# Kernel optimization log

Measured on AMD Instinct MI355X. Metric: run time of the kernel, lower is better.

## Reference

```python
import jax, jax.numpy as jnp
import numpy as np

NUM_SLOTS = 8
SLOT_DIM = 256
ITERS = 3
EPS = 1e-8
SCALE = SLOT_DIM ** -0.5


def _ln(x, g, b, eps=1e-5):
    m = jnp.mean(x, axis=-1, keepdims=True)
    v = jnp.mean(jnp.square(x - m), axis=-1, keepdims=True)
    return (x - m) * jax.lax.rsqrt(v + eps) * g + b


def setup_inputs() -> dict:
    key = jax.random.key(0)
    ks = jax.random.split(key, 16)
    b, n, c = 32, 1024, 256
    d = SLOT_DIM
    def xavier(k, shape):
        fan_in, fan_out = shape[1], shape[0]
        lim = np.sqrt(6.0 / (fan_in + fan_out))
        return jax.random.uniform(k, shape, jnp.float32, -lim, lim)
    lim_mu = np.sqrt(6.0 / (1 + d))
    return {
        "inputs": jax.random.normal(ks[0], (b, n, c), jnp.float32),
        "noise": jax.random.normal(ks[1], (b, NUM_SLOTS, d), jnp.float32),
        "slots_mu": jax.random.uniform(ks[2], (1, 1, d), jnp.float32, -lim_mu, lim_mu),
        "slots_log_sigma": jax.random.uniform(ks[3], (1, 1, d), jnp.float32, -lim_mu, lim_mu),
        "Wq": xavier(ks[4], (d, d)),
        "Wk": xavier(ks[5], (d, c)),
        "Wv": xavier(ks[6], (d, c)),
        "gru_wih": xavier(ks[7], (3 * d, d)),
        "gru_whh": xavier(ks[8], (3 * d, d)),
        "gru_bih": jnp.zeros((3 * d,), jnp.float32),
        "gru_bhh": jnp.zeros((3 * d,), jnp.float32),
        "mlp_w1": xavier(ks[9], (4 * d, d)),
        "mlp_b1": jnp.zeros((4 * d,), jnp.float32),
        "mlp_w2": xavier(ks[10], (d, 4 * d)),
        "mlp_b2": jnp.zeros((d,), jnp.float32),
        "ln_in_g": jnp.ones((c,), jnp.float32),
        "ln_in_b": jnp.zeros((c,), jnp.float32),
        "ln_s_g": jnp.ones((d,), jnp.float32),
        "ln_s_b": jnp.zeros((d,), jnp.float32),
        "ln_ff_g": jnp.ones((d,), jnp.float32),
        "ln_ff_b": jnp.zeros((d,), jnp.float32),
    }


def reference(inputs, noise, slots_mu, slots_log_sigma, Wq, Wk, Wv,
              gru_wih, gru_whh, gru_bih, gru_bhh,
              mlp_w1, mlp_b1, mlp_w2, mlp_b2,
              ln_in_g, ln_in_b, ln_s_g, ln_s_b, ln_ff_g, ln_ff_b):
    b = inputs.shape[0]
    d = SLOT_DIM
    # slots ~ N(mu, sigma) reparameterized with given noise
    slots = slots_mu + jnp.exp(slots_log_sigma) * noise  # [b, S, d]
    x = _ln(inputs, ln_in_g, ln_in_b)
    k = jnp.einsum('bnc,dc->bnd', x, Wk)
    v = jnp.einsum('bnc,dc->bnd', x, Wv)
    for _ in range(ITERS):
        slots_prev = slots
        s = _ln(slots, ln_s_g, ln_s_b)
        q = jnp.einsum('bid,ed->bie', s, Wq)
        dots = jnp.einsum('bid,bjd->bij', q, k) * SCALE  # [b, S, n]
        attn = jax.nn.softmax(dots, axis=1) + EPS         # softmax over slots
        attn = attn / jnp.sum(attn, axis=-1, keepdims=True)
        updates = jnp.einsum('bjd,bij->bid', v, attn)      # [b, S, d]
        # GRUCell: x=updates, h=slots_prev (flattened over batch*slots)
        u = updates.reshape(-1, d)
        h = slots_prev.reshape(-1, d)
        gi = u @ gru_wih.T + gru_bih
        gh = h @ gru_whh.T + gru_bhh
        i_r, i_z, i_n = jnp.split(gi, 3, axis=-1)
        h_r, h_z, h_n = jnp.split(gh, 3, axis=-1)
        r = jax.nn.sigmoid(i_r + h_r)
        z = jax.nn.sigmoid(i_z + h_z)
        nn_ = jnp.tanh(i_n + r * h_n)
        slots = ((1.0 - z) * nn_ + z * h).reshape(b, -1, d)
        ff = _ln(slots, ln_ff_g, ln_ff_b)
        ff = jax.nn.relu(ff @ mlp_w1.T + mlp_b1) @ mlp_w2.T + mlp_b2
        slots = slots + ff
    return slots
```

## Files before the change

### kernel.cpp

```cpp
#include <hip/hip_runtime.h>


typedef __attribute__((ext_vector_type(8))) __bf16 bf16x8;
typedef __attribute__((ext_vector_type(4))) float  f32x4;

#define MFMA16(a, b, c) __builtin_amdgcn_mfma_f32_16x16x32_bf16((a), (b), (c), 0, 0, 0)

static __device__ __forceinline__ unsigned short f2bf(float f) {
    unsigned int x = __float_as_uint(f);
    x = (x + 0x7fffu + ((x >> 16) & 1u)) >> 16;
    return (unsigned short)x;
}
static __device__ __forceinline__ float bf2f(unsigned short u) {
    return __uint_as_float((unsigned int)u << 16);
}
static __device__ __forceinline__ float bflo(unsigned int x) {
    return __uint_as_float(x << 16);
}
static __device__ __forceinline__ float bfhi(unsigned int x) {
    return __uint_as_float(x & 0xffff0000u);
}

struct Params {
    const float *inputs, *noise, *mu, *ls;
    const float *Wq, *Wk, *Wv, *wih, *whh, *bih, *bhh, *w1, *b1, *w2, *b2;
    const float *ln_in_g, *ln_in_b, *ln_s_g, *ln_s_b, *ln_ff_g, *ln_ff_b;
    float* out;
    unsigned short *x_bf, *kvW_bf, *Wq_bf, *wih_bf, *whh_bf, *w1_bf, *w2_bf;
    unsigned short *kv_bf, *h_bf, *ff_bf, *h1_bf;
    float *slots, *q, *upart, *rspart, *gi, *gh, *opart;
};

static __device__ void qgemm(const Params& p, const unsigned short (&u)[16][264], int r0) {
    const int t = threadIdx.x, w = t >> 6, lane = t & 63;
    const int lr = lane & 15, lq = lane >> 4;
    f32x4 acc[4] = {};
    for (int k0 = 0; k0 < 256; k0 += 32) {
        bf16x8 a = *(const bf16x8*)&u[lr][k0 + lq * 8];
        #pragma unroll
        for (int j = 0; j < 4; ++j) {
            bf16x8 bv = *(const bf16x8*)(p.Wq_bf + (size_t)(w * 64 + j * 16 + lr) * 256 + k0 + lq * 8);
            acc[j] = MFMA16(a, bv, acc[j]);
        }
    }
    #pragma unroll
    for (int j = 0; j < 4; ++j)
        #pragma unroll
        for (int r = 0; r < 4; ++r)
            p.q[(size_t)(r0 + lq * 4 + r) * 256 + w * 64 + j * 16 + lr] = acc[j][r];
}

__global__ __launch_bounds__(256) void k_prep(Params p) {
    const int bid = blockIdx.x, t = threadIdx.x;
    for (int gid = bid * 256 + t; gid < 1179648; gid += 4608 * 256) {
        if      (gid <   65536) p.kvW_bf[gid]          = f2bf(p.Wk[gid]);
        else if (gid <  131072) p.kvW_bf[gid]          = f2bf(p.Wv[gid -   65536]);
        else if (gid <  196608) p.Wq_bf[gid - 131072]  = f2bf(p.Wq[gid -  131072]);
        else if (gid <  393216) p.wih_bf[gid - 196608] = f2bf(p.wih[gid - 196608]);
        else if (gid <  589824) p.whh_bf[gid - 393216] = f2bf(p.whh[gid - 393216]);
        else if (gid <  851968) p.w1_bf[gid - 589824]  = f2bf(p.w1[gid -  589824]);
        else if (gid < 1114112) p.w2_bf[gid - 851968]  = f2bf(p.w2[gid -  851968]);
        else {
            const int i = gid - 1114112;
            const int d = i & 255;
            p.slots[i] = p.mu[d] + expf(p.ls[d]) * p.noise[i];
        }
    }
    const int wid  = (bid * 256 + t) >> 6;
    const int lane = t & 63;
    const float g0 = p.ln_in_g[lane * 4 + 0], g1 = p.ln_in_g[lane * 4 + 1];
    const float g2 = p.ln_in_g[lane * 4 + 2], g3 = p.ln_in_g[lane * 4 + 3];
    const float b0 = p.ln_in_b[lane * 4 + 0], b1 = p.ln_in_b[lane * 4 + 1];
    const float b2 = p.ln_in_b[lane * 4 + 2], b3 = p.ln_in_b[lane * 4 + 3];
    #pragma unroll 2
    for (int row = wid; row < 32768; row += 18432) {
        float4 v = *(const float4*)(p.inputs + (size_t)row * 256 + lane * 4);
        float s  = v.x + v.y + v.z + v.w;
        float ss = v.x * v.x + v.y * v.y + v.z * v.z + v.w * v.w;
        #pragma unroll
        for (int o = 1; o < 64; o <<= 1) { s += __shfl_xor(s, o); ss += __shfl_xor(ss, o); }
        float mean = s * (1.f / 256.f);
        float var  = ss * (1.f / 256.f) - mean * mean;
        float rstd = rsqrtf(var + 1e-5f);
        ushort4 o4;
        o4.x = f2bf((v.x - mean) * rstd * g0 + b0);
        o4.y = f2bf((v.y - mean) * rstd * g1 + b1);
        o4.z = f2bf((v.z - mean) * rstd * g2 + b2);
        o4.w = f2bf((v.w - mean) * rstd * g3 + b3);
        *(ushort4*)(p.x_bf + (size_t)row * 256 + lane * 4) = o4;
    }
}

union KvSmem {
    struct { unsigned short As[128 * 32], Bs[128 * 32]; } g;
    unsigned short u[16][264];
};

__global__ __launch_bounds__(256) void k_kv(Params p) {
    __shared__ KvSmem sm;
    const int bid = blockIdx.x, t = threadIdx.x;
    if (bid < 1024) {
        const int m0 = (bid >> 2) * 128, n0 = (bid & 3) * 128;
        const int wave = t >> 6, lane = t & 63;
        const int qr = (wave >> 1) * 64, qc = (wave & 1) * 64;
        const int lr = lane & 15, lq = lane >> 4;
        f32x4 acc[4][4] = {};
        const int sr = t >> 2, sl = t & 3, gk = sl * 8;
        const int wsl0 = (sl ^ ((sr >> 1) & 3)) * 8;
        const int wsl1 = (sl ^ (((sr + 64) >> 1) & 3)) * 8;
        for (int k0 = 0; k0 < 256; k0 += 32) {
            __syncthreads();
            uint4 a0 = *(const uint4*)(p.x_bf   + (size_t)(m0 + sr)      * 256 + k0 + gk);
            uint4 a1 = *(const uint4*)(p.x_bf   + (size_t)(m0 + sr + 64) * 256 + k0 + gk);
            uint4 b0 = *(const uint4*)(p.kvW_bf + (size_t)(n0 + sr)      * 256 + k0 + gk);
            uint4 b1 = *(const uint4*)(p.kvW_bf + (size_t)(n0 + sr + 64) * 256 + k0 + gk);
            *(uint4*)(sm.g.As + sr * 32 + wsl0) = a0;
            *(uint4*)(sm.g.As + (sr + 64) * 32 + wsl1) = a1;
            *(uint4*)(sm.g.Bs + sr * 32 + wsl0) = b0;
            *(uint4*)(sm.g.Bs + (sr + 64) * 32 + wsl1) = b1;
            __syncthreads();
            bf16x8 af[4], bv[4];
            #pragma unroll
            for (int i = 0; i < 4; i++) {
                const int ra = qr + i * 16 + lr;
                af[i] = *(const bf16x8*)(sm.g.As + ra * 32 + ((lq ^ ((ra >> 1) & 3)) * 8));
            }
            #pragma unroll
            for (int i = 0; i < 4; i++) {
                const int rb = qc + i * 16 + lr;
                bv[i] = *(const bf16x8*)(sm.g.Bs + rb * 32 + ((lq ^ ((rb >> 1) & 3)) * 8));
            }
            #pragma unroll
            for (int i = 0; i < 4; i++)
                #pragma unroll
                for (int j = 0; j < 4; j++)
                    acc[i][j] = MFMA16(af[i], bv[j], acc[i][j]);
        }
        #pragma unroll
        for (int i = 0; i < 4; i++)
            #pragma unroll
            for (int j = 0; j < 4; j++) {
                const int col = n0 + qc + j * 16 + lr;
                #pragma unroll
                for (int r = 0; r < 4; r++) {
                    const int rw = m0 + qr + i * 16 + lq * 4 + r;
                    p.kv_bf[(size_t)rw * 512 + col] = f2bf(acc[i][j][r]);
                }
            }
    } else {
        const int r0 = (bid - 1024) * 16;
        const int row16 = t >> 4, sub = t & 15;
        float vals[16]; float s = 0.f, ss = 0.f;
        #pragma unroll
        for (int k = 0; k < 16; k += 4) {
            float4 v = *(const float4*)(p.slots + (size_t)(r0 + row16) * 256 + sub * 16 + k);
            vals[k] = v.x; vals[k + 1] = v.y; vals[k + 2] = v.z; vals[k + 3] = v.w;
            s += v.x + v.y + v.z + v.w;
            ss += v.x * v.x + v.y * v.y + v.z * v.z + v.w * v.w;
        }
        #pragma unroll
        for (int m = 1; m < 16; m <<= 1) { s += __shfl_xor(s, m); ss += __shfl_xor(ss, m); }
        const float mean = s * (1.f / 256.f);
        const float var  = ss * (1.f / 256.f) - mean * mean;
        const float rstd = rsqrtf(var + 1e-5f);
        #pragma unroll
        for (int k = 0; k < 16; ++k) {
            const int c = sub * 16 + k;
            p.h_bf[(size_t)(r0 + row16) * 256 + c] = f2bf(vals[k]);
            sm.u[row16][c] = f2bf((vals[k] - mean) * rstd * p.ln_s_g[c] + p.ln_s_b[c]);
        }
        __syncthreads();
        qgemm(p, sm.u, r0);
    }
}

union AtSmem {
    struct { float q[8][260]; float sc[8][132]; } at;
    struct { unsigned short As[64 * 32], Bs[64 * 32]; } g;
};

__global__ __launch_bounds__(256) void k_attn_gh(Params p) {
    __shared__ AtSmem sm;
    const int bid = blockIdx.x, t = threadIdx.x;
    if (bid < 256) {
        const int b = bid >> 3, chunk = bid & 7, j0 = chunk * 128;
        {
            const int i = t >> 5, c0 = (t & 31) * 8;
            const float* qr = p.q + (size_t)(b * 8 + i) * 256 + c0;
            *(float4*)&sm.at.q[i][c0]     = *(const float4*)(qr);
            *(float4*)&sm.at.q[i][c0 + 4] = *(const float4*)(qr + 4);
        }
        __syncthreads();
        {
            const int i = t & 7, jj = t >> 3;
            const float4* qrow = (const float4*)&sm.at.q[i][0];
            #pragma unroll 1
            for (int g = 0; g < 4; ++g) {
                const int jl = g * 32 + jj;
                const uint4* krow = (const uint4*)(p.kv_bf + ((size_t)b * 1024 + j0 + jl) * 512);
                float a0 = 0, a1 = 0, a2 = 0, a3 = 0;
                #pragma unroll 8
                for (int dd = 0; dd < 32; ++dd) {
                    uint4 kk = krow[dd];
                    float4 q0 = qrow[2 * dd], q1 = qrow[2 * dd + 1];
                    a0 += q0.x * bflo(kk.x); a1 += q0.y * bfhi(kk.x);
                    a2 += q0.z * bflo(kk.y); a3 += q0.w * bfhi(kk.y);
                    a0 += q1.x * bflo(kk.z); a1 += q1.y * bfhi(kk.z);
                    a2 += q1.z * bflo(kk.w); a3 += q1.w * bfhi(kk.w);
                }
                sm.at.sc[i][jl] = (a0 + a1 + a2 + a3) * 0.0625f;
            }
        }
        __syncthreads();
        if (t < 128) {
            float v[8], m = -1e30f;
            #pragma unroll
            for (int ii = 0; ii < 8; ++ii) { v[ii] = sm.at.sc[ii][t]; m = fmaxf(m, v[ii]); }
            float s = 0.f;
            #pragma unroll
            for (int ii = 0; ii < 8; ++ii) { v[ii] = __expf(v[ii] - m); s += v[ii]; }
            const float inv = 1.f / s;
            #pragma unroll
            for (int ii = 0; ii < 8; ++ii) sm.at.sc[ii][t] = v[ii] * inv + 1e-8f;
        }
        __syncthreads();
        if (t < 8) {
            float s = 0.f;
            for (int jl = 0; jl < 128; ++jl) s += sm.at.sc[t][jl];
            p.rspart[((size_t)b * 8 + chunk) * 8 + t] = s;
        }
        {
            float acc[8] = {};
            const unsigned short* vbase = p.kv_bf + ((size_t)b * 1024 + j0) * 512 + 256 + t;
            #pragma unroll 8
            for (int jl = 0; jl < 128; ++jl) {
                const float vv = bf2f(vbase[(size_t)jl * 512]);
                #pragma unroll
                for (int ii = 0; ii < 8; ++ii) acc[ii] += sm.at.sc[ii][jl] * vv;
            }
            float* up = p.upart + (((size_t)b * 8 + chunk) * 8) * 256 + t;
            #pragma unroll
            for (int ii = 0; ii < 8; ++ii) up[ii * 256] = acc[ii];
        }
    } else {
        const int g = bid - 256;
        const int m0 = (g & 3) * 64, n0 = (g >> 2) * 64;
        const int wave = t >> 6, lane = t & 63;
        const int lr = lane & 15, lq = lane >> 4;
        f32x4 acc[4] = {};
        const int sr = t >> 2, sl = t & 3, gk = sl * 8;
        const int wsl = (sl ^ ((sr >> 1) & 3)) * 8;
        for (int k0 = 0; k0 < 256; k0 += 32) {
            __syncthreads();
            uint4 a0 = *(const uint4*)(p.h_bf   + (size_t)(m0 + sr) * 256 + k0 + gk);
            uint4 b0 = *(const uint4*)(p.whh_bf + (size_t)(n0 + sr) * 256 + k0 + gk);
            *(uint4*)(sm.g.As + sr * 32 + wsl) = a0;
            *(uint4*)(sm.g.Bs + sr * 32 + wsl) = b0;
            __syncthreads();
            const int ra = wave * 16 + lr;
            bf16x8 af = *(const bf16x8*)(sm.g.As + ra * 32 + ((lq ^ ((ra >> 1) & 3)) * 8));
            #pragma unroll
            for (int j = 0; j < 4; ++j) {
                const int rb = j * 16 + lr;
                bf16x8 bv = *(const bf16x8*)(sm.g.Bs + rb * 32 + ((lq ^ ((rb >> 1) & 3)) * 8));
                acc[j] = MFMA16(af, bv, acc[j]);
            }
        }
        #pragma unroll
        for (int j = 0; j < 4; ++j) {
            const int col = n0 + j * 16 + lr;
            #pragma unroll
            for (int r = 0; r < 4; ++r)
                p.gh[(size_t)(m0 + wave * 16 + lq * 4 + r) * 768 + col] = acc[j][r];
        }
    }
}

__global__ __launch_bounds__(256) void k_gi(Params p) {
    __shared__ unsigned short uS[8][2048];
    __shared__ unsigned short Bs[64 * 32];
    __shared__ float rs_l[64];
    const int t = threadIdx.x;
    const int m0 = blockIdx.x * 64, n0 = blockIdx.y * 64;
    if (t < 64) {
        const int grow = m0 + t, b = grow >> 3, i = grow & 7;
        float rs = 0.f;
        #pragma unroll
        for (int c = 0; c < 8; ++c) rs += p.rspart[((size_t)b * 8 + c) * 8 + i];
        rs_l[t] = 1.f / rs;
    }
    __syncthreads();
    {
        const int sl = (t >> 3) & 3, kc = t >> 5, k7 = t & 7;
        for (int r = 0; r < 64; ++r) {
            const int grow = m0 + r, b = grow >> 3, i = grow & 7;
            float a = 0.f;
            #pragma unroll
            for (int c = 0; c < 8; ++c)
                a += p.upart[(((size_t)b * 8 + c) * 8 + i) * 256 + t];
            uS[kc][r * 32 + ((sl ^ ((r >> 1) & 3)) * 8) + k7] = f2bf(a * rs_l[r]);
        }
    }
    const int wave = t >> 6, lane = t & 63;
    const int lr = lane & 15, lq = lane >> 4;
    f32x4 acc[4] = {};
    const int sr = t >> 2, sl2 = t & 3, gk = sl2 * 8;
    const int wsl = (sl2 ^ ((sr >> 1) & 3)) * 8;
    for (int k0 = 0; k0 < 256; k0 += 32) {
        __syncthreads();
        uint4 b0 = *(const uint4*)(p.wih_bf + (size_t)(n0 + sr) * 256 + k0 + gk);
        *(uint4*)(Bs + sr * 32 + wsl) = b0;
        __syncthreads();
        const int ra = wave * 16 + lr;
        bf16x8 af = *(const bf16x8*)(uS[k0 >> 5] + ra * 32 + ((lq ^ ((ra >> 1) & 3)) * 8));
        #pragma unroll
        for (int j = 0; j < 4; ++j) {
            const int rb = j * 16 + lr;
            bf16x8 bv = *(const bf16x8*)(Bs + rb * 32 + ((lq ^ ((rb >> 1) & 3)) * 8));
            acc[j] = MFMA16(af, bv, acc[j]);
        }
    }
    #pragma unroll
    for (int j = 0; j < 4; ++j) {
        const int col = n0 + j * 16 + lr;
        #pragma unroll
        for (int r = 0; r < 4; ++r)
            p.gi[(size_t)(m0 + wave * 16 + lq * 4 + r) * 768 + col] = acc[j][r];
    }
}

__global__ __launch_bounds__(256) void k_gruln(Params p) {
    __shared__ float red[8];
    const int row = blockIdx.x, t = threadIdx.x;
    const float* gir = p.gi + (size_t)row * 768;
    const float* ghr = p.gh + (size_t)row * 768;
    const float ir  = gir[t]       + p.bih[t];
    const float iz  = gir[256 + t] + p.bih[256 + t];
    const float in_ = gir[512 + t] + p.bih[512 + t];
    const float hr  = ghr[t]       + p.bhh[t];
    const float hz  = ghr[256 + t] + p.bhh[256 + t];
    const float hn  = ghr[512 + t] + p.bhh[512 + t];
    const float r = 1.f / (1.f + __expf(-(ir + hr)));
    const float z = 1.f / (1.f + __expf(-(iz + hz)));
    const float n = tanhf(in_ + r * hn);
    const float h = p.slots[(size_t)row * 256 + t];
    const float s = (1.f - z) * n + z * h;
    p.slots[(size_t)row * 256 + t] = s;
    float sm = s, ssq = s * s;
    #pragma unroll
    for (int o = 32; o > 0; o >>= 1) { sm += __shfl_down(sm, o); ssq += __shfl_down(ssq, o); }
    if ((t & 63) == 0) { red[t >> 6] = sm; red[4 + (t >> 6)] = ssq; }
    __syncthreads();
    const float S  = red[0] + red[1] + red[2] + red[3];
    const float SS = red[4] + red[5] + red[6] + red[7];
    const float mean = S * (1.f / 256.f);
    const float var  = SS * (1.f / 256.f) - mean * mean;
    const float rstd = rsqrtf(var + 1e-5f);
    p.ff_bf[(size_t)row * 256 + t] = f2bf((s - mean) * rstd * p.ln_ff_g[t] + p.ln_ff_b[t]);
}

__global__ __launch_bounds__(256) void k_mlp1(Params p) {
    __shared__ unsigned short As[64 * 32], Bs[64 * 32];
    const int m0 = blockIdx.x * 64, n0 = blockIdx.y * 64;
    const int t = threadIdx.x, wave = t >> 6, lane = t & 63;
    const int lr = lane & 15, lq = lane >> 4;
    f32x4 acc[4] = {};
    const int sr = t >> 2, sl = t & 3, gk = sl * 8;
    const int wsl = (sl ^ ((sr >> 1) & 3)) * 8;
    for (int k0 = 0; k0 < 256; k0 += 32) {
        __syncthreads();
        uint4 a0 = *(const uint4*)(p.ff_bf + (size_t)(m0 + sr) * 256 + k0 + gk);
        uint4 b0 = *(const uint4*)(p.w1_bf + (size_t)(n0 + sr) * 256 + k0 + gk);
        *(uint4*)(As + sr * 32 + wsl) = a0;
        *(uint4*)(Bs + sr * 32 + wsl) = b0;
        __syncthreads();
        const int ra = wave * 16 + lr;
        bf16x8 af = *(const bf16x8*)(As + ra * 32 + ((lq ^ ((ra >> 1) & 3)) * 8));
        #pragma unroll
        for (int j = 0; j < 4; ++j) {
            const int rb = j * 16 + lr;
            bf16x8 bv = *(const bf16x8*)(Bs + rb * 32 + ((lq ^ ((rb >> 1) & 3)) * 8));
            acc[j] = MFMA16(af, bv, acc[j]);
        }
    }
    #pragma unroll
    for (int j = 0; j < 4; ++j) {
        const int col = n0 + j * 16 + lr;
        const float bb = p.b1[col];
        #pragma unroll
        for (int r = 0; r < 4; ++r) {
            const int row = m0 + wave * 16 + lq * 4 + r;
            p.h1_bf[(size_t)row * 1024 + col] = f2bf(fmaxf(acc[j][r] + bb, 0.f));
        }
    }
}

__global__ __launch_bounds__(256) void k_out(Params p) {
    __shared__ unsigned short a_s[16][264];
    const int t = threadIdx.x;
    const int r0 = blockIdx.x * 16, kb = blockIdx.y * 256;
    const int row16 = t >> 4, sub = t & 15;
    {
        const unsigned short* src = p.h1_bf + (size_t)(r0 + row16) * 1024 + kb + sub * 16;
        *(uint4*)&a_s[row16][sub * 16]     = *(const uint4*)(src);
        *(uint4*)&a_s[row16][sub * 16 + 8] = *(const uint4*)(src + 8);
    }
    __syncthreads();
    const int w = t >> 6, lane = t & 63;
    const int lr = lane & 15, lq = lane >> 4;
    f32x4 acc[4] = {};
    for (int k0 = 0; k0 < 256; k0 += 32) {
        bf16x8 a = *(const bf16x8*)&a_s[lr][k0 + lq * 8];
        #pragma unroll
        for (int j = 0; j < 4; ++j) {
            bf16x8 bv = *(const bf16x8*)(p.w2_bf + (size_t)(w * 64 + j * 16 + lr) * 1024 + kb + k0 + lq * 8);
            acc[j] = MFMA16(a, bv, acc[j]);
        }
    }
    #pragma unroll
    for (int j = 0; j < 4; ++j)
        #pragma unroll
        for (int r = 0; r < 4; ++r)
            p.opart[((size_t)blockIdx.y * 256 + r0 + lq * 4 + r) * 256 + w * 64 + j * 16 + lr] = acc[j][r];
}

template<int LAST>
__global__ __launch_bounds__(256) void k_lnq(Params p) {
    __shared__ unsigned short u[16][264];
    const int t = threadIdx.x;
    const int r0 = blockIdx.x * 16;
    const int row16 = t >> 4, sub = t & 15;
    float vals[16]; float s_ = 0.f, ss = 0.f;
    #pragma unroll
    for (int k = 0; k < 16; ++k) {
        const int c = sub * 16 + k;
        const size_t ridx = (size_t)(r0 + row16) * 256 + c;
        float v = p.opart[(size_t)(r0 + row16) * 256 + c]
                + p.opart[((size_t)256 + r0 + row16) * 256 + c]
                + p.opart[((size_t)512 + r0 + row16) * 256 + c]
                + p.opart[((size_t)768 + r0 + row16) * 256 + c]
                + p.b2[c] + p.slots[ridx];
        if (LAST) { p.out[ridx] = v; }
        else {
            p.slots[ridx] = v;
            p.h_bf[ridx]  = f2bf(v);
        }
        vals[k] = v; s_ += v; ss += v * v;
    }
    if (LAST) return;
    #pragma unroll
    for (int m = 1; m < 16; m <<= 1) { s_ += __shfl_xor(s_, m); ss += __shfl_xor(ss, m); }
    const float mean = s_ * (1.f / 256.f);
    const float var  = ss * (1.f / 256.f) - mean * mean;
    const float rstd = rsqrtf(var + 1e-5f);
    #pragma unroll
    for (int k = 0; k < 16; ++k) {
        const int c = sub * 16 + k;
        u[row16][c] = f2bf((vals[k] - mean) * rstd * p.ln_s_g[c] + p.ln_s_b[c]);
    }
    __syncthreads();
    qgemm(p, u, r0);
}

extern "C" void kernel_launch(void* const* d_in, const int* in_sizes, int n_in,
                              void* d_out, int out_size, void* d_ws, size_t ws_size,
                              hipStream_t stream)
{
    (void)in_sizes; (void)n_in; (void)out_size; (void)ws_size;

    Params prm;
    prm.inputs  = (const float*)d_in[0];
    prm.noise   = (const float*)d_in[1];
    prm.mu      = (const float*)d_in[2];
    prm.ls      = (const float*)d_in[3];
    prm.Wq      = (const float*)d_in[4];
    prm.Wk      = (const float*)d_in[5];
    prm.Wv      = (const float*)d_in[6];
    prm.wih     = (const float*)d_in[7];
    prm.whh     = (const float*)d_in[8];
    prm.bih     = (const float*)d_in[9];
    prm.bhh     = (const float*)d_in[10];
    prm.w1      = (const float*)d_in[11];
    prm.b1      = (const float*)d_in[12];
    prm.w2      = (const float*)d_in[13];
    prm.b2      = (const float*)d_in[14];
    prm.ln_in_g = (const float*)d_in[15];
    prm.ln_in_b = (const float*)d_in[16];
    prm.ln_s_g  = (const float*)d_in[17];
    prm.ln_s_b  = (const float*)d_in[18];
    prm.ln_ff_g = (const float*)d_in[19];
    prm.ln_ff_b = (const float*)d_in[20];
    prm.out     = (float*)d_out;

    char* ptr = (char*)d_ws;
    auto alloc = [&](size_t bytes) -> char* {
        char* r = ptr; ptr += (bytes + 255) & ~(size_t)255; return r;
    };
    prm.x_bf   = (unsigned short*)alloc((size_t)32768 * 256 * 2);
    prm.kv_bf  = (unsigned short*)alloc((size_t)32768 * 512 * 2);
    prm.kvW_bf = (unsigned short*)alloc(512 * 256 * 2);
    prm.Wq_bf  = (unsigned short*)alloc(256 * 256 * 2);
    prm.wih_bf = (unsigned short*)alloc(768 * 256 * 2);
    prm.whh_bf = (unsigned short*)alloc(768 * 256 * 2);
    prm.w1_bf  = (unsigned short*)alloc(1024 * 256 * 2);
    prm.w2_bf  = (unsigned short*)alloc(256 * 1024 * 2);
    prm.slots  = (float*)         alloc(256 * 256 * 4);
    prm.q      = (float*)         alloc(256 * 256 * 4);
    prm.upart  = (float*)         alloc((size_t)32 * 8 * 8 * 256 * 4);
    prm.rspart = (float*)         alloc(32 * 8 * 8 * 4);
    prm.h_bf   = (unsigned short*)alloc(256 * 256 * 2);
    prm.gi     = (float*)         alloc(256 * 768 * 4);
    prm.gh     = (float*)         alloc(256 * 768 * 4);
    prm.ff_bf  = (unsigned short*)alloc(256 * 256 * 2);
    prm.h1_bf  = (unsigned short*)alloc(256 * 1024 * 2);
    prm.opart  = (float*)         alloc((size_t)4 * 256 * 256 * 4);

    k_prep<<<4608, 256, 0, stream>>>(prm);
    k_kv  <<<1040, 256, 0, stream>>>(prm);
    for (int it = 0; it < 3; ++it) {
        k_attn_gh<<<304, 256, 0, stream>>>(prm);
        k_gi     <<<dim3(4, 12), 256, 0, stream>>>(prm);
        k_gruln  <<<256, 256, 0, stream>>>(prm);
        k_mlp1   <<<dim3(4, 16), 256, 0, stream>>>(prm);
        k_out    <<<dim3(16, 4), 256, 0, stream>>>(prm);
        if (it < 2) k_lnq<0><<<16, 256, 0, stream>>>(prm);
        else        k_lnq<1><<<16, 256, 0, stream>>>(prm);
    }
}
```

Before: 356.9 us.

## Fuse input layernorm into KV GEMM, split attention finer, fuse GRU into MLP1

The input LayerNorm now runs inside the KV projection kernel. Each block normalizes 128 input rows straight into shared memory and loops over all 512 output columns, so the bf16 x buffer is no longer written to and read back from global memory. The attention kernel splits each batch into 16 chunks of 64 tokens instead of 8 of 128 to launch more blocks. A new kernel reduces the partial updates into bf16 before the gi GEMM, which removes the redundant reduction that k_gi's 12 column blocks each repeated. The GRU cell and FF LayerNorm are fused into the first MLP GEMM, using a separate smid buffer; this costs recomputing the GRU once per column block, and the KV kernel now uses more shared memory and fewer, longer-running blocks.

```diff
diff --git a/kernel.cpp b/kernel.cpp
--- a/kernel.cpp
+++ b/kernel.cpp
@@ -26,9 +26,9 @@
     const float *Wq, *Wk, *Wv, *wih, *whh, *bih, *bhh, *w1, *b1, *w2, *b2;
     const float *ln_in_g, *ln_in_b, *ln_s_g, *ln_s_b, *ln_ff_g, *ln_ff_b;
     float* out;
-    unsigned short *x_bf, *kvW_bf, *Wq_bf, *wih_bf, *whh_bf, *w1_bf, *w2_bf;
-    unsigned short *kv_bf, *h_bf, *ff_bf, *h1_bf;
-    float *slots, *q, *upart, *rspart, *gi, *gh, *opart;
+    unsigned short *kvW_bf, *Wq_bf, *wih_bf, *whh_bf, *w1_bf, *w2_bf;
+    unsigned short *kv_bf, *u_bf, *h_bf, *h1_bf;
+    float *slots, *smid, *q, *upart, *rspart, *gi, *gh, *opart;
 };
 
 static __device__ void qgemm(const Params& p, const unsigned short (&u)[16][264], int r0) {
@@ -51,8 +51,7 @@
 }
 
 __global__ __launch_bounds__(256) void k_prep(Params p) {
-    const int bid = blockIdx.x, t = threadIdx.x;
-    for (int gid = bid * 256 + t; gid < 1179648; gid += 4608 * 256) {
+    for (int gid = blockIdx.x * 256 + threadIdx.x; gid < 1179648; gid += 1152 * 256) {
         if      (gid <   65536) p.kvW_bf[gid]          = f2bf(p.Wk[gid]);
         else if (gid <  131072) p.kvW_bf[gid]          = f2bf(p.Wv[gid -   65536]);
         else if (gid <  196608) p.Wq_bf[gid - 131072]  = f2bf(p.Wq[gid -  131072]);
@@ -66,89 +65,88 @@
             p.slots[i] = p.mu[d] + expf(p.ls[d]) * p.noise[i];
         }
     }
-    const int wid  = (bid * 256 + t) >> 6;
-    const int lane = t & 63;
-    const float g0 = p.ln_in_g[lane * 4 + 0], g1 = p.ln_in_g[lane * 4 + 1];
-    const float g2 = p.ln_in_g[lane * 4 + 2], g3 = p.ln_in_g[lane * 4 + 3];
-    const float b0 = p.ln_in_b[lane * 4 + 0], b1 = p.ln_in_b[lane * 4 + 1];
-    const float b2 = p.ln_in_b[lane * 4 + 2], b3 = p.ln_in_b[lane * 4 + 3];
-    #pragma unroll 2
-    for (int row = wid; row < 32768; row += 18432) {
-        float4 v = *(const float4*)(p.inputs + (size_t)row * 256 + lane * 4);
-        float s  = v.x + v.y + v.z + v.w;
-        float ss = v.x * v.x + v.y * v.y + v.z * v.z + v.w * v.w;
-        #pragma unroll
-        for (int o = 1; o < 64; o <<= 1) { s += __shfl_xor(s, o); ss += __shfl_xor(ss, o); }
-        float mean = s * (1.f / 256.f);
-        float var  = ss * (1.f / 256.f) - mean * mean;
-        float rstd = rsqrtf(var + 1e-5f);
-        ushort4 o4;
-        o4.x = f2bf((v.x - mean) * rstd * g0 + b0);
-        o4.y = f2bf((v.y - mean) * rstd * g1 + b1);
-        o4.z = f2bf((v.z - mean) * rstd * g2 + b2);
-        o4.w = f2bf((v.w - mean) * rstd * g3 + b3);
-        *(ushort4*)(p.x_bf + (size_t)row * 256 + lane * 4) = o4;
-    }
 }
 
 union KvSmem {
-    struct { unsigned short As[128 * 32], Bs[128 * 32]; } g;
+    struct { unsigned short As[128 * 256]; unsigned short Bs[64 * 32]; } g;
     unsigned short u[16][264];
 };
 
 __global__ __launch_bounds__(256) void k_kv(Params p) {
     __shared__ KvSmem sm;
     const int bid = blockIdx.x, t = threadIdx.x;
-    if (bid < 1024) {
-        const int m0 = (bid >> 2) * 128, n0 = (bid & 3) * 128;
+    if (bid < 256) {
+        const int r0 = bid * 128;
         const int wave = t >> 6, lane = t & 63;
-        const int qr = (wave >> 1) * 64, qc = (wave & 1) * 64;
+        {
+            const float g0 = p.ln_in_g[lane * 4 + 0], g1 = p.ln_in_g[lane * 4 + 1];
+            const float g2 = p.ln_in_g[lane * 4 + 2], g3 = p.ln_in_g[lane * 4 + 3];
+            const float b0 = p.ln_in_b[lane * 4 + 0], b1 = p.ln_in_b[lane * 4 + 1];
+            const float b2 = p.ln_in_b[lane * 4 + 2], b3 = p.ln_in_b[lane * 4 + 3];
+            const int c = lane * 4;
+            const int chunk = c >> 5, sl = (c >> 3) & 3, c7 = c & 7;
+            for (int rr = 0; rr < 32; ++rr) {
+                const int row = rr * 4 + wave;
+                float4 v = *(const float4*)(p.inputs + (size_t)(r0 + row) * 256 + c);
+                float s  = v.x + v.y + v.z + v.w;
+                float ss = v.x * v.x + v.y * v.y + v.z * v.z + v.w * v.w;
+                #pragma unroll
+                for (int o = 1; o < 64; o <<= 1) { s += __shfl_xor(s, o); ss += __shfl_xor(ss, o); }
+                const float mean = s * (1.f / 256.f);
+                const float var  = ss * (1.f / 256.f) - mean * mean;
+                const float rstd = rsqrtf(var + 1e-5f);
+                ushort4 o4;
+                o4.x = f2bf((v.x - mean) * rstd * g0 + b0);
+                o4.y = f2bf((v.y - mean) * rstd * g1 + b1);
+                o4.z = f2bf((v.z - mean) * rstd * g2 + b2);
+                o4.w = f2bf((v.w - mean) * rstd * g3 + b3);
+                const int swz = sl ^ ((row >> 1) & 3);
+                *(ushort4*)(sm.g.As + row * 256 + chunk * 32 + swz * 8 + c7) = o4;
+            }
+        }
+        __syncthreads();
         const int lr = lane & 15, lq = lane >> 4;
-        f32x4 acc[4][4] = {};
-        const int sr = t >> 2, sl = t & 3, gk = sl * 8;
-        const int wsl0 = (sl ^ ((sr >> 1) & 3)) * 8;
-        const int wsl1 = (sl ^ (((sr + 64) >> 1) & 3)) * 8;
-        for (int k0 = 0; k0 < 256; k0 += 32) {
-            __syncthreads();
-            uint4 a0 = *(const uint4*)(p.x_bf   + (size_t)(m0 + sr)      * 256 + k0 + gk);
-            uint4 a1 = *(const uint4*)(p.x_bf   + (size_t)(m0 + sr + 64) * 256 + k0 + gk);
-            uint4 b0 = *(const uint4*)(p.kvW_bf + (size_t)(n0 + sr)      * 256 + k0 + gk);
-            uint4 b1 = *(const uint4*)(p.kvW_bf + (size_t)(n0 + sr + 64) * 256 + k0 + gk);
-            *(uint4*)(sm.g.As + sr * 32 + wsl0) = a0;
-            *(uint4*)(sm.g.As + (sr + 64) * 32 + wsl1) = a1;
-            *(uint4*)(sm.g.Bs + sr * 32 + wsl0) = b0;
-            *(uint4*)(sm.g.Bs + (sr + 64) * 32 + wsl1) = b1;
-            __syncthreads();
-            bf16x8 af[4], bv[4];
-            #pragma unroll
-            for (int i = 0; i < 4; i++) {
-                const int ra = qr + i * 16 + lr;
-                af[i] = *(const bf16x8*)(sm.g.As + ra * 32 + ((lq ^ ((ra >> 1) & 3)) * 8));
+        const int sr = t >> 2, sl2 = t & 3, gk = sl2 * 8;
+        const int wsl = (sl2 ^ ((sr >> 1) & 3)) * 8;
+        for (int nt = 0; nt < 8; ++nt) {
+            const int n0 = nt * 64;
+            f32x4 acc[2][4] = {};
+            for (int k0 = 0; k0 < 256; k0 += 32) {
+                __syncthreads();
+                uint4 b0v = *(const uint4*)(p.kvW_bf + (size_t)(n0 + sr) * 256 + k0 + gk);
+                *(uint4*)(sm.g.Bs + sr * 32 + wsl) = b0v;
+                __syncthreads();
+                bf16x8 af[2], bv[4];
+                #pragma unroll
+                for (int i = 0; i < 2; ++i) {
+                    const int ra = wave * 32 + i * 16 + lr;
+                    af[i] = *(const bf16x8*)(sm.g.As + ra * 256 + (k0 >> 5) * 32 + ((lq ^ ((ra >> 1) & 3)) * 8));
+                }
+                #pragma unroll
+                for (int j = 0; j < 4; ++j) {
+                    const int rb = j * 16 + lr;
+                    bv[j] = *(const bf16x8*)(sm.g.Bs + rb * 32 + ((lq ^ ((rb >> 1) & 3)) * 8));
+                }
+                #pragma unroll
+                for (int i = 0; i < 2; ++i)
+                    #pragma unroll
+                    for (int j = 0; j < 4; ++j)
+                        acc[i][j] = MFMA16(af[i], bv[j], acc[i][j]);
             }
             #pragma unroll
-            for (int i = 0; i < 4; i++) {
-                const int rb = qc + i * 16 + lr;
-                bv[i] = *(const bf16x8*)(sm.g.Bs + rb * 32 + ((lq ^ ((rb >> 1) & 3)) * 8));
-            }
-            #pragma unroll
-            for (int i = 0; i < 4; i++)
+            for (int i = 0; i < 2; ++i)
                 #pragma unroll
-                for (int j = 0; j < 4; j++)
-                    acc[i][j] = MFMA16(af[i], bv[j], acc[i][j]);
-        }
-        #pragma unroll
-        for (int i = 0; i < 4; i++)
-            #pragma unroll
-            for (int j = 0; j < 4; j++) {
-                const int col = n0 + qc + j * 16 + lr;
-                #pragma unroll
-                for (int r = 0; r < 4; r++) {
-                    const int rw = m0 + qr + i * 16 + lq * 4 + r;
-                    p.kv_bf[(size_t)rw * 512 + col] = f2bf(acc[i][j][r]);
+                for (int j = 0; j < 4; ++j) {
+                    const int col = n0 + j * 16 + lr;
+                    #pragma unroll
+                    for (int r = 0; r < 4; ++r) {
+                        const int rw = r0 + wave * 32 + i * 16 + lq * 4 + r;
+                        p.kv_bf[(size_t)rw * 512 + col] = f2bf(acc[i][j][r]);
+                    }
                 }
-            }
+        }
     } else {
-        const int r0 = (bid - 1024) * 16;
+        const int r0 = (bid - 256) * 16;
         const int row16 = t >> 4, sub = t & 15;
         float vals[16]; float s = 0.f, ss = 0.f;
         #pragma unroll
@@ -175,15 +173,15 @@
 }
 
 union AtSmem {
-    struct { float q[8][260]; float sc[8][132]; } at;
+    struct { float q[8][260]; float sc[8][68]; } at;
     struct { unsigned short As[64 * 32], Bs[64 * 32]; } g;
 };
 
 __global__ __launch_bounds__(256) void k_attn_gh(Params p) {
     __shared__ AtSmem sm;
     const int bid = blockIdx.x, t = threadIdx.x;
-    if (bid < 256) {
-        const int b = bid >> 3, chunk = bid & 7, j0 = chunk * 128;
+    if (bid < 512) {
+        const int b = bid >> 4, chunk = bid & 15, j0 = chunk * 64;
         {
             const int i = t >> 5, c0 = (t & 31) * 8;
             const float* qr = p.q + (size_t)(b * 8 + i) * 256 + c0;
@@ -195,7 +193,7 @@
             const int i = t & 7, jj = t >> 3;
             const float4* qrow = (const float4*)&sm.at.q[i][0];
             #pragma unroll 1
-            for (int g = 0; g < 4; ++g) {
+            for (int g = 0; g < 2; ++g) {
                 const int jl = g * 32 + jj;
                 const uint4* krow = (const uint4*)(p.kv_bf + ((size_t)b * 1024 + j0 + jl) * 512);
                 float a0 = 0, a1 = 0, a2 = 0, a3 = 0;
@@ -212,7 +210,7 @@
             }
         }
         __syncthreads();
-        if (t < 128) {
+        if (t < 64) {
             float v[8], m = -1e30f;
             #pragma unroll
             for (int ii = 0; ii < 8; ++ii) { v[ii] = sm.at.sc[ii][t]; m = fmaxf(m, v[ii]); }
@@ -226,24 +224,24 @@
         __syncthreads();
         if (t < 8) {
             float s = 0.f;
-            for (int jl = 0; jl < 128; ++jl) s += sm.at.sc[t][jl];
-            p.rspart[((size_t)b * 8 + chunk) * 8 + t] = s;
+            for (int jl = 0; jl < 64; ++jl) s += sm.at.sc[t][jl];
+            p.rspart[((size_t)b * 16 + chunk) * 8 + t] = s;
         }
         {
             float acc[8] = {};
             const unsigned short* vbase = p.kv_bf + ((size_t)b * 1024 + j0) * 512 + 256 + t;
             #pragma unroll 8
-            for (int jl = 0; jl < 128; ++jl) {
+            for (int jl = 0; jl < 64; ++jl) {
                 const float vv = bf2f(vbase[(size_t)jl * 512]);
                 #pragma unroll
                 for (int ii = 0; ii < 8; ++ii) acc[ii] += sm.at.sc[ii][jl] * vv;
             }
-            float* up = p.upart + (((size_t)b * 8 + chunk) * 8) * 256 + t;
+            float* up = p.upart + (((size_t)b * 16 + chunk) * 8) * 256 + t;
             #pragma unroll
             for (int ii = 0; ii < 8; ++ii) up[ii * 256] = acc[ii];
         }
     } else {
-        const int g = bid - 256;
+        const int g = bid - 512;
         const int m0 = (g & 3) * 64, n0 = (g >> 2) * 64;
         const int wave = t >> 6, lane = t & 63;
         const int lr = lane & 15, lq = lane >> 4;
@@ -276,90 +274,19 @@
     }
 }
 
+__global__ __launch_bounds__(256) void k_u2b(Params p) {
+    const int row = blockIdx.x, t = threadIdx.x;
+    const int b = row >> 3, i = row & 7;
+    float acc = 0.f, rs = 0.f;
+    #pragma unroll
+    for (int c = 0; c < 16; ++c) {
+        acc += p.upart[(((size_t)b * 16 + c) * 8 + i) * 256 + t];
+        rs  += p.rspart[((size_t)b * 16 + c) * 8 + i];
+    }
+    p.u_bf[(size_t)row * 256 + t] = f2bf(acc / rs);
+}
+
 __global__ __launch_bounds__(256) void k_gi(Params p) {
-    __shared__ unsigned short uS[8][2048];
-    __shared__ unsigned short Bs[64 * 32];
-    __shared__ float rs_l[64];
-    const int t = threadIdx.x;
-    const int m0 = blockIdx.x * 64, n0 = blockIdx.y * 64;
-    if (t < 64) {
-        const int grow = m0 + t, b = grow >> 3, i = grow & 7;
-        float rs = 0.f;
-        #pragma unroll
-        for (int c = 0; c < 8; ++c) rs += p.rspart[((size_t)b * 8 + c) * 8 + i];
-        rs_l[t] = 1.f / rs;
-    }
-    __syncthreads();
-    {
-        const int sl = (t >> 3) & 3, kc = t >> 5, k7 = t & 7;
-        for (int r = 0; r < 64; ++r) {
-            const int grow = m0 + r, b = grow >> 3, i = grow & 7;
-            float a = 0.f;
-            #pragma unroll
-            for (int c = 0; c < 8; ++c)
-                a += p.upart[(((size_t)b * 8 + c) * 8 + i) * 256 + t];
-            uS[kc][r * 32 + ((sl ^ ((r >> 1) & 3)) * 8) + k7] = f2bf(a * rs_l[r]);
-        }
-    }
-    const int wave = t >> 6, lane = t & 63;
-    const int lr = lane & 15, lq = lane >> 4;
-    f32x4 acc[4] = {};
-    const int sr = t >> 2, sl2 = t & 3, gk = sl2 * 8;
-    const int wsl = (sl2 ^ ((sr >> 1) & 3)) * 8;
-    for (int k0 = 0; k0 < 256; k0 += 32) {
-        __syncthreads();
-        uint4 b0 = *(const uint4*)(p.wih_bf + (size_t)(n0 + sr) * 256 + k0 + gk);
-        *(uint4*)(Bs + sr * 32 + wsl) = b0;
-        __syncthreads();
-        const int ra = wave * 16 + lr;
-        bf16x8 af = *(const bf16x8*)(uS[k0 >> 5] + ra * 32 + ((lq ^ ((ra >> 1) & 3)) * 8));
-        #pragma unroll
-        for (int j = 0; j < 4; ++j) {
-            const int rb = j * 16 + lr;
-            bf16x8 bv = *(const bf16x8*)(Bs + rb * 32 + ((lq ^ ((rb >> 1) & 3)) * 8));
-            acc[j] = MFMA16(af, bv, acc[j]);
-        }
-    }
-    #pragma unroll
-    for (int j = 0; j < 4; ++j) {
-        const int col = n0 + j * 16 + lr;
-        #pragma unroll
-        for (int r = 0; r < 4; ++r)
-            p.gi[(size_t)(m0 + wave * 16 + lq * 4 + r) * 768 + col] = acc[j][r];
-    }
-}
-
-__global__ __launch_bounds__(256) void k_gruln(Params p) {
-    __shared__ float red[8];
-    const int row = blockIdx.x, t = threadIdx.x;
-    const float* gir = p.gi + (size_t)row * 768;
-    const float* ghr = p.gh + (size_t)row * 768;
-    const float ir  = gir[t]       + p.bih[t];
-    const float iz  = gir[256 + t] + p.bih[256 + t];
-    const float in_ = gir[512 + t] + p.bih[512 + t];
-    const float hr  = ghr[t]       + p.bhh[t];
-    const float hz  = ghr[256 + t] + p.bhh[256 + t];
-    const float hn  = ghr[512 + t] + p.bhh[512 + t];
-    const float r = 1.f / (1.f + __expf(-(ir + hr)));
-    const float z = 1.f / (1.f + __expf(-(iz + hz)));
-    const float n = tanhf(in_ + r * hn);
-    const float h = p.slots[(size_t)row * 256 + t];
-    const float s = (1.f - z) * n + z * h;
-    p.slots[(size_t)row * 256 + t] = s;
-    float sm = s, ssq = s * s;
-    #pragma unroll
-    for (int o = 32; o > 0; o >>= 1) { sm += __shfl_down(sm, o); ssq += __shfl_down(ssq, o); }
-    if ((t & 63) == 0) { red[t >> 6] = sm; red[4 + (t >> 6)] = ssq; }
-    __syncthreads();
-    const float S  = red[0] + red[1] + red[2] + red[3];
-    const float SS = red[4] + red[5] + red[6] + red[7];
-    const float mean = S * (1.f / 256.f);
-    const float var  = SS * (1.f / 256.f) - mean * mean;
-    const float rstd = rsqrtf(var + 1e-5f);
-    p.ff_bf[(size_t)row * 256 + t] = f2bf((s - mean) * rstd * p.ln_ff_g[t] + p.ln_ff_b[t]);
-}
-
-__global__ __launch_bounds__(256) void k_mlp1(Params p) {
     __shared__ unsigned short As[64 * 32], Bs[64 * 32];
     const int m0 = blockIdx.x * 64, n0 = blockIdx.y * 64;
     const int t = threadIdx.x, wave = t >> 6, lane = t & 63;
@@ -369,8 +296,8 @@
     const int wsl = (sl ^ ((sr >> 1) & 3)) * 8;
     for (int k0 = 0; k0 < 256; k0 += 32) {
         __syncthreads();
-        uint4 a0 = *(const uint4*)(p.ff_bf + (size_t)(m0 + sr) * 256 + k0 + gk);
-        uint4 b0 = *(const uint4*)(p.w1_bf + (size_t)(n0 + sr) * 256 + k0 + gk);
+        uint4 a0 = *(const uint4*)(p.u_bf   + (size_t)(m0 + sr) * 256 + k0 + gk);
+        uint4 b0 = *(const uint4*)(p.wih_bf + (size_t)(n0 + sr) * 256 + k0 + gk);
         *(uint4*)(As + sr * 32 + wsl) = a0;
         *(uint4*)(Bs + sr * 32 + wsl) = b0;
         __syncthreads();
@@ -386,12 +313,66 @@
     #pragma unroll
     for (int j = 0; j < 4; ++j) {
         const int col = n0 + j * 16 + lr;
+        #pragma unroll
+        for (int r = 0; r < 4; ++r)
+            p.gi[(size_t)(m0 + wave * 16 + lq * 4 + r) * 768 + col] = acc[j][r];
+    }
+}
+
+__global__ __launch_bounds__(256) void k_mlp1f(Params p) {
+    __shared__ unsigned short ff[16][264];
+    const int t = threadIdx.x;
+    const int r0 = blockIdx.x * 16, nb = blockIdx.y * 256;
+    const int row16 = t >> 4, sub = t & 15;
+    const int grow = r0 + row16;
+    const float* gir = p.gi + (size_t)grow * 768;
+    const float* ghr = p.gh + (size_t)grow * 768;
+    float vals[16]; float s_ = 0.f, ss = 0.f;
+    #pragma unroll
+    for (int k = 0; k < 16; ++k) {
+        const int c = sub * 16 + k;
+        const float ir  = gir[c]       + p.bih[c];
+        const float iz  = gir[256 + c] + p.bih[256 + c];
+        const float in_ = gir[512 + c] + p.bih[512 + c];
+        const float hr  = ghr[c]       + p.bhh[c];
+        const float hz  = ghr[256 + c] + p.bhh[256 + c];
+        const float hn  = ghr[512 + c] + p.bhh[512 + c];
+        const float r = 1.f / (1.f + __expf(-(ir + hr)));
+        const float z = 1.f / (1.f + __expf(-(iz + hz)));
+        const float n = tanhf(in_ + r * hn);
+        const float h = p.slots[(size_t)grow * 256 + c];
+        const float s = (1.f - z) * n + z * h;
+        if (blockIdx.y == 0) p.smid[(size_t)grow * 256 + c] = s;
+        vals[k] = s; s_ += s; ss += s * s;
+    }
+    #pragma unroll
+    for (int m = 1; m < 16; m <<= 1) { s_ += __shfl_xor(s_, m); ss += __shfl_xor(ss, m); }
+    const float mean = s_ * (1.f / 256.f);
+    const float var  = ss * (1.f / 256.f) - mean * mean;
+    const float rstd = rsqrtf(var + 1e-5f);
+    #pragma unroll
+    for (int k = 0; k < 16; ++k) {
+        const int c = sub * 16 + k;
+        ff[row16][c] = f2bf((vals[k] - mean) * rstd * p.ln_ff_g[c] + p.ln_ff_b[c]);
+    }
+    __syncthreads();
+    const int w = t >> 6, lane = t & 63, lr = lane & 15, lq = lane >> 4;
+    f32x4 acc[4] = {};
+    for (int k0 = 0; k0 < 256; k0 += 32) {
+        bf16x8 a = *(const bf16x8*)&ff[lr][k0 + lq * 8];
+        #pragma unroll
+        for (int j = 0; j < 4; ++j) {
+            bf16x8 bv = *(const bf16x8*)(p.w1_bf + (size_t)(nb + w * 64 + j * 16 + lr) * 256 + k0 + lq * 8);
+            acc[j] = MFMA16(a, bv, acc[j]);
+        }
+    }
+    #pragma unroll
+    for (int j = 0; j < 4; ++j) {
+        const int col = nb + w * 64 + j * 16 + lr;
         const float bb = p.b1[col];
         #pragma unroll
-        for (int r = 0; r < 4; ++r) {
-            const int row = m0 + wave * 16 + lq * 4 + r;
-            p.h1_bf[(size_t)row * 1024 + col] = f2bf(fmaxf(acc[j][r] + bb, 0.f));
-        }
+        for (int r = 0; r < 4; ++r)
+            p.h1_bf[(size_t)(r0 + lq * 4 + r) * 1024 + col] = f2bf(fmaxf(acc[j][r] + bb, 0.f));
     }
 }
 
@@ -439,7 +420,7 @@
                 + p.opart[((size_t)256 + r0 + row16) * 256 + c]
                 + p.opart[((size_t)512 + r0 + row16) * 256 + c]
                 + p.opart[((size_t)768 + r0 + row16) * 256 + c]
-                + p.b2[c] + p.slots[ridx];
+                + p.b2[c] + p.smid[ridx];
         if (LAST) { p.out[ridx] = v; }
         else {
             p.slots[ridx] = v;
@@ -496,7 +477,6 @@
     auto alloc = [&](size_t bytes) -> char* {
         char* r = ptr; ptr += (bytes + 255) & ~(size_t)255; return r;
     };
-    prm.x_bf   = (unsigned short*)alloc((size_t)32768 * 256 * 2);
     prm.kv_bf  = (unsigned short*)alloc((size_t)32768 * 512 * 2);
     prm.kvW_bf = (unsigned short*)alloc(512 * 256 * 2);
     prm.Wq_bf  = (unsigned short*)alloc(256 * 256 * 2);
@@ -505,23 +485,24 @@
     prm.w1_bf  = (unsigned short*)alloc(1024 * 256 * 2);
     prm.w2_bf  = (unsigned short*)alloc(256 * 1024 * 2);
     prm.slots  = (float*)         alloc(256 * 256 * 4);
+    prm.smid   = (float*)         alloc(256 * 256 * 4);
     prm.q      = (float*)         alloc(256 * 256 * 4);
-    prm.upart  = (float*)         alloc((size_t)32 * 8 * 8 * 256 * 4);
-    prm.rspart = (float*)         alloc(32 * 8 * 8 * 4);
+    prm.upart  = (float*)         alloc((size_t)32 * 16 * 8 * 256 * 4);
+    prm.rspart = (float*)         alloc(32 * 16 * 8 * 4);
+    prm.u_bf   = (unsigned short*)alloc(256 * 256 * 2);
     prm.h_bf   = (unsigned short*)alloc(256 * 256 * 2);
     prm.gi     = (float*)         alloc(256 * 768 * 4);
     prm.gh     = (float*)         alloc(256 * 768 * 4);
-    prm.ff_bf  = (unsigned short*)alloc(256 * 256 * 2);
     prm.h1_bf  = (unsigned short*)alloc(256 * 1024 * 2);
     prm.opart  = (float*)         alloc((size_t)4 * 256 * 256 * 4);
 
-    k_prep<<<4608, 256, 0, stream>>>(prm);
-    k_kv  <<<1040, 256, 0, stream>>>(prm);
+    k_prep<<<1152, 256, 0, stream>>>(prm);
+    k_kv  <<<272, 256, 0, stream>>>(prm);
     for (int it = 0; it < 3; ++it) {
-        k_attn_gh<<<304, 256, 0, stream>>>(prm);
+        k_attn_gh<<<560, 256, 0, stream>>>(prm);
+        k_u2b    <<<256, 256, 0, stream>>>(prm);
         k_gi     <<<dim3(4, 12), 256, 0, stream>>>(prm);
-        k_gruln  <<<256, 256, 0, stream>>>(prm);
-        k_mlp1   <<<dim3(4, 16), 256, 0, stream>>>(prm);
+        k_mlp1f  <<<dim3(16, 4), 256, 0, stream>>>(prm);
         k_out    <<<dim3(16, 4), 256, 0, stream>>>(prm);
         if (it < 2) k_lnq<0><<<16, 256, 0, stream>>>(prm);
         else        k_lnq<1><<<16, 256, 0, stream>>>(prm);
```

Result: slower. 392.5 us (+10.0%).
